# Kernel optimization log

Measured on AMD Instinct MI355X. Metric: run time of the kernel, lower is better.

The kernel has to match this reference:

```python
import jax, jax.numpy as jnp
import numpy as np

NUM_HEADS = 16
KEY_SIZE = 64
VALUE_SIZE = 64
D_MODEL = 1024
B, S = 2, 2048

def setup_inputs() -> dict:
    key = jax.random.key(0)
    k1, k2 = jax.random.split(key)
    inputs = jax.random.normal(k1, (B, S, D_MODEL), dtype=jnp.float32)
    qkv_width = NUM_HEADS * (KEY_SIZE + KEY_SIZE + VALUE_SIZE)  # 3072
    W = jax.random.normal(k2, (D_MODEL, qkv_width), dtype=jnp.float32) / np.sqrt(D_MODEL)
    b = jnp.zeros((qkv_width,), dtype=jnp.float32)
    return {"inputs": inputs, "W": W, "b": b}

def reference(inputs, W, b):
    # Fused QKV projection: [B, S, H*(2k+v)]
    qkv = jnp.einsum("bsd,de->bse", inputs, W) + b
    Bsz, S_ = inputs.shape[0], inputs.shape[1]
    qkv = qkv.reshape(Bsz, S_, NUM_HEADS, 2 * KEY_SIZE + VALUE_SIZE)
    qkv = jnp.transpose(qkv, (0, 2, 1, 3))  # [B, H, S, 2k+v]
    q = qkv[..., :KEY_SIZE]
    k = qkv[..., KEY_SIZE:2 * KEY_SIZE]
    v = qkv[..., 2 * KEY_SIZE:]
    # NOTE: original multiplies by sqrt(key_size) (not divide) -- faithful.
    scores = jnp.einsum("bhqd,bhkd->bhqk", q, k) * jnp.sqrt(jnp.float32(KEY_SIZE))
    weights = jax.nn.softmax(scores, axis=-1)
    out = jnp.einsum("bhqk,bhkv->bhqv", weights, v)  # [B, H, S, v]
    out = jnp.transpose(out, (0, 2, 1, 3)).reshape(Bsz, S_, NUM_HEADS * VALUE_SIZE)
    return out
```

## Files before the change

kernel.cpp:

```cpp
#include <hip/hip_runtime.h>


#define S_LEN 2048
#define NH    16
#define DH    64
#define DM    1024
#define EW    3072
#define NROWS 4096
#define NT    32

#define QSCALE 11.5415603f

using f32x4 = __attribute__((ext_vector_type(4))) float;
using bf8   = __attribute__((ext_vector_type(8))) short;
using s4v   = __attribute__((ext_vector_type(4))) short;

static __device__ __forceinline__ short f2bf(float f) {
  union { float f; unsigned u; } a; a.f = f;
  unsigned r = a.u + 0x7fffu + ((a.u >> 16) & 1u);
  return (short)(r >> 16);
}
static __device__ __forceinline__ float bf2f(short h) {
  union { float f; unsigned u; } a;
  a.u = ((unsigned)(unsigned short)h) << 16;
  return a.f;
}
static __device__ __forceinline__ void gl16(const void* g, void* l) {
  __builtin_amdgcn_global_load_lds(
      (const __attribute__((address_space(1))) void*)g,
      (__attribute__((address_space(3))) void*)l, 16, 0, 0);
}

__global__ __launch_bounds__(256) void prep_x(const float* __restrict__ X,
                                              short* __restrict__ Xh,
                                              short* __restrict__ Xl) {
  int i = blockIdx.x * 256 + threadIdx.x;
  float4 v = ((const float4*)X)[i];
  s4v h, l;
  h.x = f2bf(v.x); l.x = f2bf(v.x - bf2f(h.x));
  h.y = f2bf(v.y); l.y = f2bf(v.y - bf2f(h.y));
  h.z = f2bf(v.z); l.z = f2bf(v.z - bf2f(h.z));
  h.w = f2bf(v.w); l.w = f2bf(v.w - bf2f(h.w));
  ((s4v*)Xh)[i] = h;
  ((s4v*)Xl)[i] = l;
}

__global__ __launch_bounds__(256) void prep_w(const float* __restrict__ W,
                                              short* __restrict__ Wfh,
                                              short* __restrict__ Wfl) {
  __shared__ float t[32][33];
  int n0 = blockIdx.x * 32;
  int k0 = blockIdx.y * 32;
  int tx = threadIdx.x & 31;
  int ty = threadIdx.x >> 5;
#pragma unroll
  for (int i = 0; i < 32; i += 8)
    t[ty + i][tx] = W[(size_t)(k0 + ty + i) * EW + n0 + tx];
  __syncthreads();
  const int kt = k0 >> 5;
#pragma unroll
  for (int i = 0; i < 32; i += 8) {
    float v = t[tx][ty + i];
    int n = n0 + ty + i;
    int h = n / 192, e = n - h * 192;
    int np = (e < 64) ? (h * 64 + e)
           : (e < 128) ? (1024 + h * 64 + (e - 64))
                       : (2048 + h * 64 + (e - 128));
    int n16 = np >> 4, c = np & 15;
    int gg = (tx >> 3) & 3, ee = tx & 7;
    size_t o = ((size_t)(n16 * 32 + kt)) * 512 + (gg * 16 + c) * 8 + ee;
    short hi = f2bf(v);
    Wfh[o] = hi;
    if (np < 2048) Wfl[o] = f2bf(v - bf2f(hi));
  }
}

__global__ __launch_bounds__(256, 2) void proj_qk(
    const short* __restrict__ Xh, const short* __restrict__ Xl,
    const short* __restrict__ Wfh, const short* __restrict__ Wfl,
    const float* __restrict__ bias,
    short* __restrict__ Qh, short* __restrict__ Ql,
    short* __restrict__ Kh, short* __restrict__ Kl) {
  __shared__ short Ah[2][4096], Al[2][4096];
  const int tid = threadIdx.x;
  const int lane = tid & 63, w = tid >> 6;
  const int wr = w >> 1, wc = w & 1;
  const int c = lane & 15, g = lane >> 4;

  const int id = blockIdx.x;
  const int t = id >> 3;
  const int rowBase = (((id & 7) << 2) + (t & 3)) * 128;
  const int colBase = (t >> 2) * 128;

  f32x4 acc[4][4] = {};

  const int sr  = 32 * w + (lane >> 2);
  const int csw = ((lane & 3) ^ ((lane >> 3) & 3)) * 8;
  const int ldsw = w * 1024;
  const size_t aBase = (size_t)(rowBase + sr) * DM + csw;
  const int rsw = (g ^ ((c >> 1) & 3)) * 8;

  size_t bB[4];
#pragma unroll
  for (int n = 0; n < 4; ++n)
    bB[n] = ((size_t)((colBase >> 4) + wc * 4 + n) * 32) * 512 + lane * 8;

#define ASTAGE(B, kt) do {                                    \
    gl16(&Xh[aBase + (kt)],            &Ah[B][ldsw]);         \
    gl16(&Xh[aBase + (kt) + 16 * DM],  &Ah[B][ldsw + 512]);   \
    gl16(&Xl[aBase + (kt)],            &Al[B][ldsw]);         \
    gl16(&Xl[aBase + (kt) + 16 * DM],  &Al[B][ldsw + 512]);   \
  } while (0)
#define LOADB(dh, dl, kt) do {                                \
    _Pragma("unroll")                                         \
    for (int n = 0; n < 4; ++n) {                             \
      dh[n] = *(const bf8*)&Wfh[bB[n] + (size_t)(kt) * 512];  \
      dl[n] = *(const bf8*)&Wfl[bB[n] + (size_t)(kt) * 512];  \
    }                                                         \
  } while (0)
#define QKMFMA(bh, bl) do {                                   \
    _Pragma("unroll")                                         \
    for (int m = 0; m < 4; ++m) {                             \
      _Pragma("unroll")                                       \
      for (int n = 0; n < 4; ++n) {                           \
        acc[m][n] = __builtin_amdgcn_mfma_f32_16x16x32_bf16(al4[m], bh[n], acc[m][n], 0, 0, 0); \
        acc[m][n] = __builtin_amdgcn_mfma_f32_16x16x32_bf16(ah[m], bl[n], acc[m][n], 0, 0, 0);  \
        acc[m][n] = __builtin_amdgcn_mfma_f32_16x16x32_bf16(ah[m], bh[n], acc[m][n], 0, 0, 0);  \
      }                                                       \
    }                                                         \
  } while (0)

  bf8 b0h[4], b0l[4], b1h[4], b1l[4];
  LOADB(b0h, b0l, 0);
  ASTAGE(0, 0);
  __syncthreads();

  for (int it = 0; it < 32; it += 2) {
    LOADB(b1h, b1l, it + 1);
    bf8 ah[4], al4[4];
#pragma unroll
    for (int m = 0; m < 4; ++m) {
      int ro = (wr * 64 + m * 16 + c) * 32 + rsw;
      ah[m]  = *(const bf8*)&Ah[0][ro];
      al4[m] = *(const bf8*)&Al[0][ro];
    }
    ASTAGE(1, (it + 1) * 32);
    __builtin_amdgcn_s_setprio(1);
    QKMFMA(b0h, b0l);
    __builtin_amdgcn_s_setprio(0);
    __syncthreads();

    if (it + 2 < 32) LOADB(b0h, b0l, it + 2);
#pragma unroll
    for (int m = 0; m < 4; ++m) {
      int ro = (wr * 64 + m * 16 + c) * 32 + rsw;
      ah[m]  = *(const bf8*)&Ah[1][ro];
      al4[m] = *(const bf8*)&Al[1][ro];
    }
    if (it + 2 < 32) ASTAGE(0, (it + 2) * 32);
    __builtin_amdgcn_s_setprio(1);
    QKMFMA(b1h, b1l);
    __builtin_amdgcn_s_setprio(0);
    __syncthreads();
  }
#undef ASTAGE
#undef LOADB
#undef QKMFMA

#pragma unroll
  for (int m = 0; m < 4; ++m)
#pragma unroll
    for (int n = 0; n < 4; ++n)
#pragma unroll
      for (int j = 0; j < 4; ++j) {
        int grow = rowBase + wr * 64 + m * 16 + g * 4 + j;
        int gcol = colBase + wc * 64 + n * 16 + c;
        int h = (gcol >> 6) & 15, e = gcol & 63;
        int bb = grow >> 11, s = grow & 2047;
        size_t hb = (size_t)(bb * NH + h);
        if (gcol < 1024) {
          float q8 = (acc[m][n][j] + bias[h * 192 + e]) * QSCALE;
          short hi = f2bf(q8);
          short lo = f2bf(q8 - bf2f(hi));
          size_t idx = (hb * S_LEN + s) * DH + e;
          Qh[idx] = hi; Ql[idx] = lo;
        } else {
          float v = acc[m][n][j] + bias[h * 192 + 64 + e];
          short hi = f2bf(v);
          short lo = f2bf(v - bf2f(hi));
          int tile = s >> 6, r = s & 63;
          size_t idx = ((hb * NT + tile) * (size_t)4096) + r * 64 +
                       ((((e >> 3) ^ (r & 7)) << 3) | (e & 7));
          Kh[idx] = hi; Kl[idx] = lo;
        }
      }
}

__global__ __launch_bounds__(256, 2) void proj_v(
    const short* __restrict__ Xh, const short* __restrict__ Wfh,
    const float* __restrict__ bias, short* __restrict__ Vt) {
  __shared__ short Ah[2][4096];
  const int tid = threadIdx.x;
  const int lane = tid & 63, w = tid >> 6;
  const int wr = w >> 1, wc = w & 1;
  const int c = lane & 15, g = lane >> 4;

  const int id = blockIdx.x;
  const int t = id >> 3;
  const int rowBase = (((id & 7) << 2) + (t & 3)) * 128;
  const int colBase = 2048 + (t >> 2) * 128;

  f32x4 acc[4][4] = {};

  const int sr  = 32 * w + (lane >> 2);
  const int csw = ((lane & 3) ^ ((lane >> 3) & 3)) * 8;
  const int ldsw = w * 1024;
  const size_t aBase = (size_t)(rowBase + sr) * DM + csw;
  const int rsw = (g ^ ((c >> 1) & 3)) * 8;

  size_t bB[4];
#pragma unroll
  for (int n = 0; n < 4; ++n)
    bB[n] = ((size_t)((colBase >> 4) + wc * 4 + n) * 32) * 512 + lane * 8;

#define VASTAGE(B, kt) do {                                   \
    gl16(&Xh[aBase + (kt)],            &Ah[B][ldsw]);         \
    gl16(&Xh[aBase + (kt) + 16 * DM],  &Ah[B][ldsw + 512]);   \
  } while (0)
#define VLOADB(dh, kt) do {                                   \
    _Pragma("unroll")                                         \
    for (int n = 0; n < 4; ++n)                               \
      dh[n] = *(const bf8*)&Wfh[bB[n] + (size_t)(kt) * 512];  \
  } while (0)

  bf8 b0h[4], b1h[4];
  VLOADB(b0h, 0);
  VASTAGE(0, 0);
  __syncthreads();

  for (int it = 0; it < 32; it += 2) {
    VLOADB(b1h, it + 1);
    bf8 ah[4];
#pragma unroll
    for (int m = 0; m < 4; ++m)
      ah[m] = *(const bf8*)&Ah[0][(wr * 64 + m * 16 + c) * 32 + rsw];
    VASTAGE(1, (it + 1) * 32);
    __builtin_amdgcn_s_setprio(1);
#pragma unroll
    for (int m = 0; m < 4; ++m)
#pragma unroll
      for (int n = 0; n < 4; ++n)
        acc[m][n] = __builtin_amdgcn_mfma_f32_16x16x32_bf16(ah[m], b0h[n], acc[m][n], 0, 0, 0);
    __builtin_amdgcn_s_setprio(0);
    __syncthreads();

    if (it + 2 < 32) VLOADB(b0h, it + 2);
#pragma unroll
    for (int m = 0; m < 4; ++m)
      ah[m] = *(const bf8*)&Ah[1][(wr * 64 + m * 16 + c) * 32 + rsw];
    if (it + 2 < 32) VASTAGE(0, (it + 2) * 32);
    __builtin_amdgcn_s_setprio(1);
#pragma unroll
    for (int m = 0; m < 4; ++m)
#pragma unroll
      for (int n = 0; n < 4; ++n)
        acc[m][n] = __builtin_amdgcn_mfma_f32_16x16x32_bf16(ah[m], b1h[n], acc[m][n], 0, 0, 0);
    __builtin_amdgcn_s_setprio(0);
    __syncthreads();
  }
#undef VASTAGE
#undef VLOADB

#pragma unroll
  for (int m = 0; m < 4; ++m)
#pragma unroll
    for (int n = 0; n < 4; ++n)
#pragma unroll
      for (int j = 0; j < 4; ++j) {
        int grow = rowBase + wr * 64 + m * 16 + g * 4 + j;
        int gcol = colBase + wc * 64 + n * 16 + c;
        int h = (gcol >> 6) & 15, d = gcol & 63;
        int bb = grow >> 11, s = grow & 2047;
        size_t hb = (size_t)(bb * NH + h);
        float v = acc[m][n][j] + bias[h * 192 + 128 + d];
        int tile = s >> 6, key = s & 63;
        int kc = key >> 5, g4 = (key >> 2) & 3;
        int ii = (((key >> 4) & 1) << 2) | (key & 3);
        size_t idx = ((hb * NT + tile) * (size_t)4096) + d * 64 +
                     (((((kc << 2) | g4) ^ (d & 7)) << 3) | ii);
        Vt[idx] = f2bf(v);
      }
}

__global__ __launch_bounds__(512, 4) void attn(
    const short* __restrict__ Qh, const short* __restrict__ Ql,
    const short* __restrict__ KhG, const short* __restrict__ KlG,
    const short* __restrict__ VtG, float* __restrict__ out) {
  __shared__ short KHs[2][4096];
  __shared__ short KLs[2][4096];
  __shared__ short Vs[2][4096];

  const int tid = threadIdx.x;
  const int lane = tid & 63, w = tid >> 6;
  const int c = lane & 15, g = lane >> 4;
  const int id = blockIdx.x;
  const int lid = (id & 7) * 64 + (id >> 3);
  const int bh = lid >> 4;
  const int q0 = (lid & 15) * 128 + w * 16;
  const size_t qBase  = (size_t)bh * S_LEN * DH;
  const size_t kvBase = (size_t)bh * NT * 4096;

  const int seg = tid * 8;

  bf8 qh[2], ql[2];
#pragma unroll
  for (int kc = 0; kc < 2; ++kc) {
    size_t idx = qBase + (size_t)(q0 + c) * DH + kc * 32 + g * 8;
    qh[kc] = *(const bf8*)&Qh[idx];
    ql[kc] = *(const bf8*)&Ql[idx];
  }

  int koff[2][4];
#pragma unroll
  for (int kc = 0; kc < 2; ++kc)
#pragma unroll
    for (int i = 0; i < 4; ++i)
      koff[kc][i] = (i * 16 + c) * 64 + (((kc * 4 + g) ^ (c & 7)) << 3);

  f32x4 mneg = {0.f, 0.f, 0.f, 0.f};
  f32x4 osum = {};
  f32x4 o[4] = {};
  union { bf8 v; unsigned u[4]; } ones;
  ones.u[0] = ones.u[1] = ones.u[2] = ones.u[3] = 0x3F803F80u;

  gl16(&KhG[kvBase + seg], &KHs[0][seg]);
  gl16(&KlG[kvBase + seg], &KLs[0][seg]);
  gl16(&VtG[kvBase + seg], &Vs[0][seg]);
  __syncthreads();

  for (int t = 0; t < NT; ++t) {
    const int cur = t & 1, nxt = cur ^ 1;
    if (t + 1 < NT) {
      size_t tb = kvBase + (size_t)(t + 1) * 4096 + seg;
      gl16(&KhG[tb], &KHs[nxt][seg]);
      gl16(&KlG[tb], &KLs[nxt][seg]);
      gl16(&VtG[tb], &Vs[nxt][seg]);
    }
    const short* KH = &KHs[cur][0];
    const short* KL = &KLs[cur][0];
    const short* VV = &Vs[cur][0];

    f32x4 sc[4];
    __builtin_amdgcn_s_setprio(1);
#pragma unroll
    for (int nb = 0; nb < 4; ++nb) {
      bf8 kh0 = *(const bf8*)&KH[koff[0][nb]];
      bf8 kl0 = *(const bf8*)&KL[koff[0][nb]];
      f32x4 s = __builtin_amdgcn_mfma_f32_16x16x32_bf16(kh0, ql[0], mneg, 0, 0, 0);
      s = __builtin_amdgcn_mfma_f32_16x16x32_bf16(kl0, qh[0], s, 0, 0, 0);
      s = __builtin_amdgcn_mfma_f32_16x16x32_bf16(kh0, qh[0], s, 0, 0, 0);
      bf8 kh1 = *(const bf8*)&KH[koff[1][nb]];
      bf8 kl1 = *(const bf8*)&KL[koff[1][nb]];
      s = __builtin_amdgcn_mfma_f32_16x16x32_bf16(kh1, ql[1], s, 0, 0, 0);
      s = __builtin_amdgcn_mfma_f32_16x16x32_bf16(kl1, qh[1], s, 0, 0, 0);
      s = __builtin_amdgcn_mfma_f32_16x16x32_bf16(kh1, qh[1], s, 0, 0, 0);
      sc[nb] = s;
    }
    __builtin_amdgcn_s_setprio(0);

    float m0 = fmaxf(fmaxf(sc[0][0], sc[0][1]), sc[0][2]);
    m0 = fmaxf(fmaxf(m0, sc[0][3]), sc[1][0]);
    m0 = fmaxf(fmaxf(m0, sc[1][1]), sc[1][2]);
    m0 = fmaxf(fmaxf(m0, sc[1][3]), sc[2][0]);
    m0 = fmaxf(fmaxf(m0, sc[2][1]), sc[2][2]);
    m0 = fmaxf(fmaxf(m0, sc[2][3]), sc[3][0]);
    m0 = fmaxf(fmaxf(m0, sc[3][1]), sc[3][2]);
    m0 = fmaxf(m0, sc[3][3]);
    m0 = fmaxf(m0, __shfl_xor(m0, 16));
    m0 = fmaxf(m0, __shfl_xor(m0, 32));

    if (__any(m0 > 8.0f)) {
      float delta = fmaxf(m0, 0.0f);
      float scale = exp2f(-delta);
      int sb = (g << 4) | (g << 2);
      float s0 = __shfl(scale, sb);
      float s1 = __shfl(scale, sb + 1);
      float s2 = __shfl(scale, sb + 2);
      float s3 = __shfl(scale, sb + 3);
#pragma unroll
      for (int db = 0; db < 4; ++db) {
        o[db][0] *= s0; o[db][1] *= s1; o[db][2] *= s2; o[db][3] *= s3;
      }
      osum[0] *= s0; osum[1] *= s1; osum[2] *= s2; osum[3] *= s3;
      mneg[0] -= delta; mneg[1] -= delta; mneg[2] -= delta; mneg[3] -= delta;
#pragma unroll
      for (int nb = 0; nb < 4; ++nb)
#pragma unroll
        for (int j = 0; j < 4; ++j)
          sc[nb][j] = exp2f(sc[nb][j] - delta);
    } else {
#pragma unroll
      for (int nb = 0; nb < 4; ++nb)
#pragma unroll
        for (int j = 0; j < 4; ++j)
          sc[nb][j] = exp2f(sc[nb][j]);
    }

    union { bf8 v; unsigned u[4]; } pa[2];
#pragma unroll
    for (int kc = 0; kc < 2; ++kc) {
      asm("v_cvt_pk_bf16_f32 %0, %1, %2"
          : "=v"(pa[kc].u[0]) : "v"(sc[2 * kc][0]), "v"(sc[2 * kc][1]));
      asm("v_cvt_pk_bf16_f32 %0, %1, %2"
          : "=v"(pa[kc].u[1]) : "v"(sc[2 * kc][2]), "v"(sc[2 * kc][3]));
      asm("v_cvt_pk_bf16_f32 %0, %1, %2"
          : "=v"(pa[kc].u[2]) : "v"(sc[2 * kc + 1][0]), "v"(sc[2 * kc + 1][1]));
      asm("v_cvt_pk_bf16_f32 %0, %1, %2"
          : "=v"(pa[kc].u[3]) : "v"(sc[2 * kc + 1][2]), "v"(sc[2 * kc + 1][3]));
    }

    __builtin_amdgcn_s_setprio(1);
#pragma unroll
    for (int kc = 0; kc < 2; ++kc) {
      osum = __builtin_amdgcn_mfma_f32_16x16x32_bf16(pa[kc].v, ones.v, osum, 0, 0, 0);
#pragma unroll
      for (int db = 0; db < 4; ++db) {
        bf8 vb = *(const bf8*)&VV[koff[kc][db]];
        o[db] = __builtin_amdgcn_mfma_f32_16x16x32_bf16(pa[kc].v, vb, o[db], 0, 0, 0);
      }
    }
    __builtin_amdgcn_s_setprio(0);

    __syncthreads();
  }

  float r0 = 1.f / osum[0];
  float r1 = 1.f / osum[1];
  float r2 = 1.f / osum[2];
  float r3 = 1.f / osum[3];

  const int b = bh >> 4, h = bh & 15;
#pragma unroll
  for (int db = 0; db < 4; ++db) {
    int col = h * DH + db * 16 + c;
    out[((size_t)b * S_LEN + q0 + g * 4 + 0) * DM + col] = o[db][0] * r0;
    out[((size_t)b * S_LEN + q0 + g * 4 + 1) * DM + col] = o[db][1] * r1;
    out[((size_t)b * S_LEN + q0 + g * 4 + 2) * DM + col] = o[db][2] * r2;
    out[((size_t)b * S_LEN + q0 + g * 4 + 3) * DM + col] = o[db][3] * r3;
  }
}

extern "C" void kernel_launch(void* const* d_in, const int* in_sizes, int n_in,
                              void* d_out, int out_size, void* d_ws, size_t ws_size,
                              hipStream_t stream) {
  const float* X    = (const float*)d_in[0];
  const float* W    = (const float*)d_in[1];
  const float* bias = (const float*)d_in[2];
  float* out = (float*)d_out;

  char* ws = (char*)d_ws;
  size_t off = 0;
  auto take = [&](size_t bytes) {
    void* p = ws + off;
    off += (bytes + 255) & ~(size_t)255;
    return p;
  };
  short* Xh  = (short*)take((size_t)NROWS * DM * 2);
  short* Xl  = (short*)take((size_t)NROWS * DM * 2);
  short* Wfh = (short*)take((size_t)EW * DM * 2);
  short* Wfl = (short*)take((size_t)EW * DM * 2);
  short* Qh  = (short*)take((size_t)2 * NH * S_LEN * DH * 2);
  short* Ql  = (short*)take((size_t)2 * NH * S_LEN * DH * 2);
  short* Kh  = (short*)take((size_t)2 * NH * NT * 4096 * 2);
  short* Kl  = (short*)take((size_t)2 * NH * NT * 4096 * 2);
  short* Vt  = (short*)take((size_t)2 * NH * NT * 4096 * 2);

  prep_x<<<dim3(4096), dim3(256), 0, stream>>>(X, Xh, Xl);
  prep_w<<<dim3(EW / 32, DM / 32), dim3(256), 0, stream>>>(W, Wfh, Wfl);
  proj_qk<<<dim3(512), dim3(256), 0, stream>>>(
      Xh, Xl, Wfh, Wfl, bias, Qh, Ql, Kh, Kl);
  proj_v<<<dim3(256), dim3(256), 0, stream>>>(Xh, Wfh, bias, Vt);
  attn<<<dim3(512), dim3(512), 0, stream>>>(
      Qh, Ql, Kh, Kl, Vt, out);
}
```

Measured before the change: 174.4 us.

## Merge QK and V projections into one launch; load V directly from global

```diff
diff --git a/kernel.cpp b/kernel.cpp
--- a/kernel.cpp
+++ b/kernel.cpp
@@ -75,35 +75,37 @@
   }
 }
 
-__global__ __launch_bounds__(256, 2) void proj_qk(
+__global__ __launch_bounds__(256, 2) void proj(
     const short* __restrict__ Xh, const short* __restrict__ Xl,
     const short* __restrict__ Wfh, const short* __restrict__ Wfl,
     const float* __restrict__ bias,
     short* __restrict__ Qh, short* __restrict__ Ql,
-    short* __restrict__ Kh, short* __restrict__ Kl) {
+    short* __restrict__ Kh, short* __restrict__ Kl,
+    short* __restrict__ Vt) {
   __shared__ short Ah[2][4096], Al[2][4096];
   const int tid = threadIdx.x;
   const int lane = tid & 63, w = tid >> 6;
   const int wr = w >> 1, wc = w & 1;
   const int c = lane & 15, g = lane >> 4;
 
-  const int id = blockIdx.x;
-  const int t = id >> 3;
-  const int rowBase = (((id & 7) << 2) + (t & 3)) * 128;
-  const int colBase = (t >> 2) * 128;
-
-  f32x4 acc[4][4] = {};
-
   const int sr  = 32 * w + (lane >> 2);
   const int csw = ((lane & 3) ^ ((lane >> 3) & 3)) * 8;
   const int ldsw = w * 1024;
-  const size_t aBase = (size_t)(rowBase + sr) * DM + csw;
   const int rsw = (g ^ ((c >> 1) & 3)) * 8;
 
-  size_t bB[4];
-#pragma unroll
-  for (int n = 0; n < 4; ++n)
-    bB[n] = ((size_t)((colBase >> 4) + wc * 4 + n) * 32) * 512 + lane * 8;
+  if (blockIdx.x < 512) {
+    const int id = blockIdx.x;
+    const int t = id >> 3;
+    const int rowBase = (((id & 7) << 2) + (t & 3)) * 128;
+    const int colBase = (t >> 2) * 128;
+
+    f32x4 acc[4][4] = {};
+    const size_t aBase = (size_t)(rowBase + sr) * DM + csw;
+
+    size_t bB[4];
+#pragma unroll
+    for (int n = 0; n < 4; ++n)
+      bB[n] = ((size_t)((colBase >> 4) + wc * 4 + n) * 32) * 512 + lane * 8;
 
 #define ASTAGE(B, kt) do {                                    \
     gl16(&Xh[aBase + (kt)],            &Ah[B][ldsw]);         \
@@ -130,98 +132,83 @@
     }                                                         \
   } while (0)
 
-  bf8 b0h[4], b0l[4], b1h[4], b1l[4];
-  LOADB(b0h, b0l, 0);
-  ASTAGE(0, 0);
-  __syncthreads();
-
-  for (int it = 0; it < 32; it += 2) {
-    LOADB(b1h, b1l, it + 1);
-    bf8 ah[4], al4[4];
-#pragma unroll
-    for (int m = 0; m < 4; ++m) {
-      int ro = (wr * 64 + m * 16 + c) * 32 + rsw;
-      ah[m]  = *(const bf8*)&Ah[0][ro];
-      al4[m] = *(const bf8*)&Al[0][ro];
-    }
-    ASTAGE(1, (it + 1) * 32);
-    __builtin_amdgcn_s_setprio(1);
-    QKMFMA(b0h, b0l);
-    __builtin_amdgcn_s_setprio(0);
+    bf8 b0h[4], b0l[4], b1h[4], b1l[4];
+    LOADB(b0h, b0l, 0);
+    ASTAGE(0, 0);
     __syncthreads();
 
-    if (it + 2 < 32) LOADB(b0h, b0l, it + 2);
-#pragma unroll
-    for (int m = 0; m < 4; ++m) {
-      int ro = (wr * 64 + m * 16 + c) * 32 + rsw;
-      ah[m]  = *(const bf8*)&Ah[1][ro];
-      al4[m] = *(const bf8*)&Al[1][ro];
-    }
-    if (it + 2 < 32) ASTAGE(0, (it + 2) * 32);
-    __builtin_amdgcn_s_setprio(1);
-    QKMFMA(b1h, b1l);
-    __builtin_amdgcn_s_setprio(0);
-    __syncthreads();
-  }
+    for (int it = 0; it < 32; it += 2) {
+      LOADB(b1h, b1l, it + 1);
+      bf8 ah[4], al4[4];
+#pragma unroll
+      for (int m = 0; m < 4; ++m) {
+        int ro = (wr * 64 + m * 16 + c) * 32 + rsw;
+        ah[m]  = *(const bf8*)&Ah[0][ro];
+        al4[m] = *(const bf8*)&Al[0][ro];
+      }
+      ASTAGE(1, (it + 1) * 32);
+      __builtin_amdgcn_s_setprio(1);
+      QKMFMA(b0h, b0l);
+      __builtin_amdgcn_s_setprio(0);
+      __syncthreads();
+
+      if (it + 2 < 32) LOADB(b0h, b0l, it + 2);
+#pragma unroll
+      for (int m = 0; m < 4; ++m) {
+        int ro = (wr * 64 + m * 16 + c) * 32 + rsw;
+        ah[m]  = *(const bf8*)&Ah[1][ro];
+        al4[m] = *(const bf8*)&Al[1][ro];
+      }
+      if (it + 2 < 32) ASTAGE(0, (it + 2) * 32);
+      __builtin_amdgcn_s_setprio(1);
+      QKMFMA(b1h, b1l);
+      __builtin_amdgcn_s_setprio(0);
+      __syncthreads();
+    }
 #undef ASTAGE
 #undef LOADB
 #undef QKMFMA
 
 #pragma unroll
-  for (int m = 0; m < 4; ++m)
+    for (int m = 0; m < 4; ++m)
+#pragma unroll
+      for (int n = 0; n < 4; ++n)
+#pragma unroll
+        for (int j = 0; j < 4; ++j) {
+          int grow = rowBase + wr * 64 + m * 16 + g * 4 + j;
+          int gcol = colBase + wc * 64 + n * 16 + c;
+          int h = (gcol >> 6) & 15, e = gcol & 63;
+          int bb = grow >> 11, s = grow & 2047;
+          size_t hb = (size_t)(bb * NH + h);
+          if (gcol < 1024) {
+            float q8 = (acc[m][n][j] + bias[h * 192 + e]) * QSCALE;
+            short hi = f2bf(q8);
+            short lo = f2bf(q8 - bf2f(hi));
+            size_t idx = (hb * S_LEN + s) * DH + e;
+            Qh[idx] = hi; Ql[idx] = lo;
+          } else {
+            float v = acc[m][n][j] + bias[h * 192 + 64 + e];
+            short hi = f2bf(v);
+            short lo = f2bf(v - bf2f(hi));
+            int tile = s >> 6, r = s & 63;
+            size_t idx = ((hb * NT + tile) * (size_t)4096) + r * 64 +
+                         ((((e >> 3) ^ (r & 7)) << 3) | (e & 7));
+            Kh[idx] = hi; Kl[idx] = lo;
+          }
+        }
+  } else {
+    const int id = blockIdx.x - 512;
+    const int t = id >> 3;
+    const int rowBase = (((id & 7) << 2) + (t & 3)) * 128;
+    const int colBase = 2048 + (t >> 2) * 128;
+
+    f32x4 acc[4][4] = {};
+    const size_t aBase = (size_t)(rowBase + sr) * DM + csw;
+
+    size_t bB[4];
 #pragma unroll
     for (int n = 0; n < 4; ++n)
-#pragma unroll
-      for (int j = 0; j < 4; ++j) {
-        int grow = rowBase + wr * 64 + m * 16 + g * 4 + j;
-        int gcol = colBase + wc * 64 + n * 16 + c;
-        int h = (gcol >> 6) & 15, e = gcol & 63;
-        int bb = grow >> 11, s = grow & 2047;
-        size_t hb = (size_t)(bb * NH + h);
-        if (gcol < 1024) {
-          float q8 = (acc[m][n][j] + bias[h * 192 + e]) * QSCALE;
-          short hi = f2bf(q8);
-          short lo = f2bf(q8 - bf2f(hi));
-          size_t idx = (hb * S_LEN + s) * DH + e;
-          Qh[idx] = hi; Ql[idx] = lo;
-        } else {
-          float v = acc[m][n][j] + bias[h * 192 + 64 + e];
-          short hi = f2bf(v);
-          short lo = f2bf(v - bf2f(hi));
-          int tile = s >> 6, r = s & 63;
-          size_t idx = ((hb * NT + tile) * (size_t)4096) + r * 64 +
-                       ((((e >> 3) ^ (r & 7)) << 3) | (e & 7));
-          Kh[idx] = hi; Kl[idx] = lo;
-        }
-      }
-}
-
-__global__ __launch_bounds__(256, 2) void proj_v(
-    const short* __restrict__ Xh, const short* __restrict__ Wfh,
-    const float* __restrict__ bias, short* __restrict__ Vt) {
-  __shared__ short Ah[2][4096];
-  const int tid = threadIdx.x;
-  const int lane = tid & 63, w = tid >> 6;
-  const int wr = w >> 1, wc = w & 1;
-  const int c = lane & 15, g = lane >> 4;
-
-  const int id = blockIdx.x;
-  const int t = id >> 3;
-  const int rowBase = (((id & 7) << 2) + (t & 3)) * 128;
-  const int colBase = 2048 + (t >> 2) * 128;
-
-  f32x4 acc[4][4] = {};
-
-  const int sr  = 32 * w + (lane >> 2);
-  const int csw = ((lane & 3) ^ ((lane >> 3) & 3)) * 8;
-  const int ldsw = w * 1024;
-  const size_t aBase = (size_t)(rowBase + sr) * DM + csw;
-  const int rsw = (g ^ ((c >> 1) & 3)) * 8;
-
-  size_t bB[4];
-#pragma unroll
-  for (int n = 0; n < 4; ++n)
-    bB[n] = ((size_t)((colBase >> 4) + wc * 4 + n) * 32) * 512 + lane * 8;
+      bB[n] = ((size_t)((colBase >> 4) + wc * 4 + n) * 32) * 512 + lane * 8;
 
 #define VASTAGE(B, kt) do {                                   \
     gl16(&Xh[aBase + (kt)],            &Ah[B][ldsw]);         \
@@ -233,63 +220,64 @@
       dh[n] = *(const bf8*)&Wfh[bB[n] + (size_t)(kt) * 512];  \
   } while (0)
 
-  bf8 b0h[4], b1h[4];
-  VLOADB(b0h, 0);
-  VASTAGE(0, 0);
-  __syncthreads();
-
-  for (int it = 0; it < 32; it += 2) {
-    VLOADB(b1h, it + 1);
-    bf8 ah[4];
-#pragma unroll
-    for (int m = 0; m < 4; ++m)
-      ah[m] = *(const bf8*)&Ah[0][(wr * 64 + m * 16 + c) * 32 + rsw];
-    VASTAGE(1, (it + 1) * 32);
-    __builtin_amdgcn_s_setprio(1);
-#pragma unroll
-    for (int m = 0; m < 4; ++m)
-#pragma unroll
-      for (int n = 0; n < 4; ++n)
-        acc[m][n] = __builtin_amdgcn_mfma_f32_16x16x32_bf16(ah[m], b0h[n], acc[m][n], 0, 0, 0);
-    __builtin_amdgcn_s_setprio(0);
+    bf8 b0h[4], b1h[4];
+    VLOADB(b0h, 0);
+    VASTAGE(0, 0);
     __syncthreads();
 
-    if (it + 2 < 32) VLOADB(b0h, it + 2);
-#pragma unroll
-    for (int m = 0; m < 4; ++m)
-      ah[m] = *(const bf8*)&Ah[1][(wr * 64 + m * 16 + c) * 32 + rsw];
-    if (it + 2 < 32) VASTAGE(0, (it + 2) * 32);
-    __builtin_amdgcn_s_setprio(1);
-#pragma unroll
-    for (int m = 0; m < 4; ++m)
-#pragma unroll
-      for (int n = 0; n < 4; ++n)
-        acc[m][n] = __builtin_amdgcn_mfma_f32_16x16x32_bf16(ah[m], b1h[n], acc[m][n], 0, 0, 0);
-    __builtin_amdgcn_s_setprio(0);
-    __syncthreads();
-  }
+    for (int it = 0; it < 32; it += 2) {
+      VLOADB(b1h, it + 1);
+      bf8 ah[4];
+#pragma unroll
+      for (int m = 0; m < 4; ++m)
+        ah[m] = *(const bf8*)&Ah[0][(wr * 64 + m * 16 + c) * 32 + rsw];
+      VASTAGE(1, (it + 1) * 32);
+      __builtin_amdgcn_s_setprio(1);
+#pragma unroll
+      for (int m = 0; m < 4; ++m)
+#pragma unroll
+        for (int n = 0; n < 4; ++n)
+          acc[m][n] = __builtin_amdgcn_mfma_f32_16x16x32_bf16(ah[m], b0h[n], acc[m][n], 0, 0, 0);
+      __builtin_amdgcn_s_setprio(0);
+      __syncthreads();
+
+      if (it + 2 < 32) VLOADB(b0h, it + 2);
+#pragma unroll
+      for (int m = 0; m < 4; ++m)
+        ah[m] = *(const bf8*)&Ah[1][(wr * 64 + m * 16 + c) * 32 + rsw];
+      if (it + 2 < 32) VASTAGE(0, (it + 2) * 32);
+      __builtin_amdgcn_s_setprio(1);
+#pragma unroll
+      for (int m = 0; m < 4; ++m)
+#pragma unroll
+        for (int n = 0; n < 4; ++n)
+          acc[m][n] = __builtin_amdgcn_mfma_f32_16x16x32_bf16(ah[m], b1h[n], acc[m][n], 0, 0, 0);
+      __builtin_amdgcn_s_setprio(0);
+      __syncthreads();
+    }
 #undef VASTAGE
 #undef VLOADB
 
 #pragma unroll
-  for (int m = 0; m < 4; ++m)
-#pragma unroll
-    for (int n = 0; n < 4; ++n)
-#pragma unroll
-      for (int j = 0; j < 4; ++j) {
-        int grow = rowBase + wr * 64 + m * 16 + g * 4 + j;
-        int gcol = colBase + wc * 64 + n * 16 + c;
-        int h = (gcol >> 6) & 15, d = gcol & 63;
-        int bb = grow >> 11, s = grow & 2047;
-        size_t hb = (size_t)(bb * NH + h);
-        float v = acc[m][n][j] + bias[h * 192 + 128 + d];
-        int tile = s >> 6, key = s & 63;
-        int kc = key >> 5, g4 = (key >> 2) & 3;
-        int ii = (((key >> 4) & 1) << 2) | (key & 3);
-        size_t idx = ((hb * NT + tile) * (size_t)4096) + d * 64 +
-                     (((((kc << 2) | g4) ^ (d & 7)) << 3) | ii);
-        Vt[idx] = f2bf(v);
-      }
+    for (int m = 0; m < 4; ++m)
+#pragma unroll
+      for (int n = 0; n < 4; ++n)
+#pragma unroll
+        for (int j = 0; j < 4; ++j) {
+          int grow = rowBase + wr * 64 + m * 16 + g * 4 + j;
+          int gcol = colBase + wc * 64 + n * 16 + c;
+          int h = (gcol >> 6) & 15, d = gcol & 63;
+          int bb = grow >> 11, s = grow & 2047;
+          size_t hb = (size_t)(bb * NH + h);
+          float v = acc[m][n][j] + bias[h * 192 + 128 + d];
+          int tile = s >> 6, key = s & 63;
+          int kc = key >> 5, g4 = (key >> 2) & 3;
+          int ii = (((key >> 4) & 1) << 2) | (key & 3);
+          size_t idx = ((hb * NT + tile) * (size_t)4096) + d * 64 +
+                       ((((kc << 2) | g4) << 3) | ii);
+          Vt[idx] = f2bf(v);
+        }
+  }
 }
 
 __global__ __launch_bounds__(512, 4) void attn(
@@ -298,7 +286,6 @@
     const short* __restrict__ VtG, float* __restrict__ out) {
   __shared__ short KHs[2][4096];
   __shared__ short KLs[2][4096];
-  __shared__ short Vs[2][4096];
 
   const int tid = threadIdx.x;
   const int lane = tid & 63, w = tid >> 6;
@@ -327,6 +314,13 @@
     for (int i = 0; i < 4; ++i)
       koff[kc][i] = (i * 16 + c) * 64 + (((kc * 4 + g) ^ (c & 7)) << 3);
 
+  int voff[2][4];
+#pragma unroll
+  for (int kc = 0; kc < 2; ++kc)
+#pragma unroll
+    for (int db = 0; db < 4; ++db)
+      voff[kc][db] = (db * 16 + c) * 64 + (kc * 4 + g) * 8;
+
   f32x4 mneg = {0.f, 0.f, 0.f, 0.f};
   f32x4 osum = {};
   f32x4 o[4] = {};
@@ -335,20 +329,26 @@
 
   gl16(&KhG[kvBase + seg], &KHs[0][seg]);
   gl16(&KlG[kvBase + seg], &KLs[0][seg]);
-  gl16(&VtG[kvBase + seg], &Vs[0][seg]);
   __syncthreads();
 
   for (int t = 0; t < NT; ++t) {
     const int cur = t & 1, nxt = cur ^ 1;
+    const size_t vtb = kvBase + (size_t)t * 4096;
+
+    bf8 vb[2][4];
+#pragma unroll
+    for (int kc = 0; kc < 2; ++kc)
+#pragma unroll
+      for (int db = 0; db < 4; ++db)
+        vb[kc][db] = *(const bf8*)&VtG[vtb + voff[kc][db]];
+
     if (t + 1 < NT) {
       size_t tb = kvBase + (size_t)(t + 1) * 4096 + seg;
       gl16(&KhG[tb], &KHs[nxt][seg]);
       gl16(&KlG[tb], &KLs[nxt][seg]);
-      gl16(&VtG[tb], &Vs[nxt][seg]);
     }
     const short* KH = &KHs[cur][0];
     const short* KL = &KLs[cur][0];
-    const short* VV = &Vs[cur][0];
 
     f32x4 sc[4];
     __builtin_amdgcn_s_setprio(1);
@@ -424,10 +424,8 @@
     for (int kc = 0; kc < 2; ++kc) {
       osum = __builtin_amdgcn_mfma_f32_16x16x32_bf16(pa[kc].v, ones.v, osum, 0, 0, 0);
 #pragma unroll
-      for (int db = 0; db < 4; ++db) {
-        bf8 vb = *(const bf8*)&VV[koff[kc][db]];
-        o[db] = __builtin_amdgcn_mfma_f32_16x16x32_bf16(pa[kc].v, vb, o[db], 0, 0, 0);
-      }
+      for (int db = 0; db < 4; ++db)
+        o[db] = __builtin_amdgcn_mfma_f32_16x16x32_bf16(pa[kc].v, vb[kc][db], o[db], 0, 0, 0);
     }
     __builtin_amdgcn_s_setprio(0);
 
@@ -477,9 +475,8 @@
 
   prep_x<<<dim3(4096), dim3(256), 0, stream>>>(X, Xh, Xl);
   prep_w<<<dim3(EW / 32, DM / 32), dim3(256), 0, stream>>>(W, Wfh, Wfl);
-  proj_qk<<<dim3(512), dim3(256), 0, stream>>>(
-      Xh, Xl, Wfh, Wfl, bias, Qh, Ql, Kh, Kl);
-  proj_v<<<dim3(256), dim3(256), 0, stream>>>(Xh, Wfh, bias, Vt);
+  proj<<<dim3(768), dim3(256), 0, stream>>>(
+      Xh, Xl, Wfh, Wfl, bias, Qh, Ql, Kh, Kl, Vt);
   attn<<<dim3(512), dim3(512), 0, stream>>>(
       Qh, Ql, Kh, Kl, Vt, out);
 }
```

After: 328.7 us. 88.5% more time.

## Process two 16-row query blocks per wave in attention to reuse K/V tiles

Applied to the files above, without the earlier changes.

```diff
diff --git a/kernel.cpp b/kernel.cpp
--- a/kernel.cpp
+++ b/kernel.cpp
@@ -292,7 +292,7 @@
       }
 }
 
-__global__ __launch_bounds__(512, 4) void attn(
+__global__ __launch_bounds__(512, 2) void attn(
     const short* __restrict__ Qh, const short* __restrict__ Ql,
     const short* __restrict__ KhG, const short* __restrict__ KlG,
     const short* __restrict__ VtG, float* __restrict__ out) {
@@ -304,21 +304,23 @@
   const int lane = tid & 63, w = tid >> 6;
   const int c = lane & 15, g = lane >> 4;
   const int id = blockIdx.x;
-  const int lid = (id & 7) * 64 + (id >> 3);
-  const int bh = lid >> 4;
-  const int q0 = (lid & 15) * 128 + w * 16;
+  const int lid = (id & 7) * 32 + (id >> 3);
+  const int bh = lid >> 3;
+  const int q0 = (lid & 7) * 256 + w * 32;
   const size_t qBase  = (size_t)bh * S_LEN * DH;
   const size_t kvBase = (size_t)bh * NT * 4096;
 
   const int seg = tid * 8;
 
-  bf8 qh[2], ql[2];
-#pragma unroll
-  for (int kc = 0; kc < 2; ++kc) {
-    size_t idx = qBase + (size_t)(q0 + c) * DH + kc * 32 + g * 8;
-    qh[kc] = *(const bf8*)&Qh[idx];
-    ql[kc] = *(const bf8*)&Ql[idx];
-  }
+  bf8 qh[2][2], ql[2][2];
+#pragma unroll
+  for (int rb = 0; rb < 2; ++rb)
+#pragma unroll
+    for (int kc = 0; kc < 2; ++kc) {
+      size_t idx = qBase + (size_t)(q0 + rb * 16 + c) * DH + kc * 32 + g * 8;
+      qh[rb][kc] = *(const bf8*)&Qh[idx];
+      ql[rb][kc] = *(const bf8*)&Ql[idx];
+    }
 
   int koff[2][4];
 #pragma unroll
@@ -327,9 +329,9 @@
     for (int i = 0; i < 4; ++i)
       koff[kc][i] = (i * 16 + c) * 64 + (((kc * 4 + g) ^ (c & 7)) << 3);
 
-  f32x4 mneg = {0.f, 0.f, 0.f, 0.f};
-  f32x4 osum = {};
-  f32x4 o[4] = {};
+  f32x4 mneg0 = {0.f, 0.f, 0.f, 0.f}, mneg1 = {0.f, 0.f, 0.f, 0.f};
+  f32x4 osum0 = {}, osum1 = {};
+  f32x4 o0[4] = {}, o1[4] = {};
   union { bf8 v; unsigned u[4]; } ones;
   ones.u[0] = ones.u[1] = ones.u[2] = ones.u[3] = 0x3F803F80u;
 
@@ -350,83 +352,132 @@
     const short* KL = &KLs[cur][0];
     const short* VV = &Vs[cur][0];
 
-    f32x4 sc[4];
+    f32x4 sc0[4], sc1[4];
     __builtin_amdgcn_s_setprio(1);
 #pragma unroll
     for (int nb = 0; nb < 4; ++nb) {
       bf8 kh0 = *(const bf8*)&KH[koff[0][nb]];
       bf8 kl0 = *(const bf8*)&KL[koff[0][nb]];
-      f32x4 s = __builtin_amdgcn_mfma_f32_16x16x32_bf16(kh0, ql[0], mneg, 0, 0, 0);
-      s = __builtin_amdgcn_mfma_f32_16x16x32_bf16(kl0, qh[0], s, 0, 0, 0);
-      s = __builtin_amdgcn_mfma_f32_16x16x32_bf16(kh0, qh[0], s, 0, 0, 0);
+      f32x4 s0 = __builtin_amdgcn_mfma_f32_16x16x32_bf16(kh0, ql[0][0], mneg0, 0, 0, 0);
+      s0 = __builtin_amdgcn_mfma_f32_16x16x32_bf16(kl0, qh[0][0], s0, 0, 0, 0);
+      s0 = __builtin_amdgcn_mfma_f32_16x16x32_bf16(kh0, qh[0][0], s0, 0, 0, 0);
+      f32x4 s1 = __builtin_amdgcn_mfma_f32_16x16x32_bf16(kh0, ql[1][0], mneg1, 0, 0, 0);
+      s1 = __builtin_amdgcn_mfma_f32_16x16x32_bf16(kl0, qh[1][0], s1, 0, 0, 0);
+      s1 = __builtin_amdgcn_mfma_f32_16x16x32_bf16(kh0, qh[1][0], s1, 0, 0, 0);
       bf8 kh1 = *(const bf8*)&KH[koff[1][nb]];
       bf8 kl1 = *(const bf8*)&KL[koff[1][nb]];
-      s = __builtin_amdgcn_mfma_f32_16x16x32_bf16(kh1, ql[1], s, 0, 0, 0);
-      s = __builtin_amdgcn_mfma_f32_16x16x32_bf16(kl1, qh[1], s, 0, 0, 0);
-      s = __builtin_amdgcn_mfma_f32_16x16x32_bf16(kh1, qh[1], s, 0, 0, 0);
-      sc[nb] = s;
+      s0 = __builtin_amdgcn_mfma_f32_16x16x32_bf16(kh1, ql[0][1], s0, 0, 0, 0);
+      s0 = __builtin_amdgcn_mfma_f32_16x16x32_bf16(kl1, qh[0][1], s0, 0, 0, 0);
+      s0 = __builtin_amdgcn_mfma_f32_16x16x32_bf16(kh1, qh[0][1], s0, 0, 0, 0);
+      s1 = __builtin_amdgcn_mfma_f32_16x16x32_bf16(kh1, ql[1][1], s1, 0, 0, 0);
+      s1 = __builtin_amdgcn_mfma_f32_16x16x32_bf16(kl1, qh[1][1], s1, 0, 0, 0);
+      s1 = __builtin_amdgcn_mfma_f32_16x16x32_bf16(kh1, qh[1][1], s1, 0, 0, 0);
+      sc0[nb] = s0; sc1[nb] = s1;
     }
     __builtin_amdgcn_s_setprio(0);
 
-    float m0 = fmaxf(fmaxf(sc[0][0], sc[0][1]), sc[0][2]);
-    m0 = fmaxf(fmaxf(m0, sc[0][3]), sc[1][0]);
-    m0 = fmaxf(fmaxf(m0, sc[1][1]), sc[1][2]);
-    m0 = fmaxf(fmaxf(m0, sc[1][3]), sc[2][0]);
-    m0 = fmaxf(fmaxf(m0, sc[2][1]), sc[2][2]);
-    m0 = fmaxf(fmaxf(m0, sc[2][3]), sc[3][0]);
-    m0 = fmaxf(fmaxf(m0, sc[3][1]), sc[3][2]);
-    m0 = fmaxf(m0, sc[3][3]);
-    m0 = fmaxf(m0, __shfl_xor(m0, 16));
-    m0 = fmaxf(m0, __shfl_xor(m0, 32));
-
-    if (__any(m0 > 8.0f)) {
-      float delta = fmaxf(m0, 0.0f);
-      float scale = exp2f(-delta);
+    float m00 = fmaxf(fmaxf(sc0[0][0], sc0[0][1]), sc0[0][2]);
+    m00 = fmaxf(fmaxf(m00, sc0[0][3]), sc0[1][0]);
+    m00 = fmaxf(fmaxf(m00, sc0[1][1]), sc0[1][2]);
+    m00 = fmaxf(fmaxf(m00, sc0[1][3]), sc0[2][0]);
+    m00 = fmaxf(fmaxf(m00, sc0[2][1]), sc0[2][2]);
+    m00 = fmaxf(fmaxf(m00, sc0[2][3]), sc0[3][0]);
+    m00 = fmaxf(fmaxf(m00, sc0[3][1]), sc0[3][2]);
+    m00 = fmaxf(m00, sc0[3][3]);
+    m00 = fmaxf(m00, __shfl_xor(m00, 16));
+    m00 = fmaxf(m00, __shfl_xor(m00, 32));
+    float m01 = fmaxf(fmaxf(sc1[0][0], sc1[0][1]), sc1[0][2]);
+    m01 = fmaxf(fmaxf(m01, sc1[0][3]), sc1[1][0]);
+    m01 = fmaxf(fmaxf(m01, sc1[1][1]), sc1[1][2]);
+    m01 = fmaxf(fmaxf(m01, sc1[1][3]), sc1[2][0]);
+    m01 = fmaxf(fmaxf(m01, sc1[2][1]), sc1[2][2]);
+    m01 = fmaxf(fmaxf(m01, sc1[2][3]), sc1[3][0]);
+    m01 = fmaxf(fmaxf(m01, sc1[3][1]), sc1[3][2]);
+    m01 = fmaxf(m01, sc1[3][3]);
+    m01 = fmaxf(m01, __shfl_xor(m01, 16));
+    m01 = fmaxf(m01, __shfl_xor(m01, 32));
+
+    if (__any(fmaxf(m00, m01) > 8.0f)) {
       int sb = (g << 4) | (g << 2);
-      float s0 = __shfl(scale, sb);
-      float s1 = __shfl(scale, sb + 1);
-      float s2 = __shfl(scale, sb + 2);
-      float s3 = __shfl(scale, sb + 3);
-#pragma unroll
-      for (int db = 0; db < 4; ++db) {
-        o[db][0] *= s0; o[db][1] *= s1; o[db][2] *= s2; o[db][3] *= s3;
+      {
+        float delta = fmaxf(m00, 0.0f);
+        float scale = exp2f(-delta);
+        float s0 = __shfl(scale, sb);
+        float s1 = __shfl(scale, sb + 1);
+        float s2 = __shfl(scale, sb + 2);
+        float s3 = __shfl(scale, sb + 3);
+#pragma unroll
+        for (int db = 0; db < 4; ++db) {
+          o0[db][0] *= s0; o0[db][1] *= s1; o0[db][2] *= s2; o0[db][3] *= s3;
+        }
+        osum0[0] *= s0; osum0[1] *= s1; osum0[2] *= s2; osum0[3] *= s3;
+        mneg0[0] -= delta; mneg0[1] -= delta; mneg0[2] -= delta; mneg0[3] -= delta;
+#pragma unroll
+        for (int nb = 0; nb < 4; ++nb)
+#pragma unroll
+          for (int j = 0; j < 4; ++j)
+            sc0[nb][j] = exp2f(sc0[nb][j] - delta);
       }
-      osum[0] *= s0; osum[1] *= s1; osum[2] *= s2; osum[3] *= s3;
-      mneg[0] -= delta; mneg[1] -= delta; mneg[2] -= delta; mneg[3] -= delta;
+      {
+        float delta = fmaxf(m01, 0.0f);
+        float scale = exp2f(-delta);
+        float s0 = __shfl(scale, sb);
+        float s1 = __shfl(scale, sb + 1);
+        float s2 = __shfl(scale, sb + 2);
+        float s3 = __shfl(scale, sb + 3);
+#pragma unroll
+        for (int db = 0; db < 4; ++db) {
+          o1[db][0] *= s0; o1[db][1] *= s1; o1[db][2] *= s2; o1[db][3] *= s3;
+        }
+        osum1[0] *= s0; osum1[1] *= s1; osum1[2] *= s2; osum1[3] *= s3;
+        mneg1[0] -= delta; mneg1[1] -= delta; mneg1[2] -= delta; mneg1[3] -= delta;
+#pragma unroll
+        for (int nb = 0; nb < 4; ++nb)
+#pragma unroll
+          for (int j = 0; j < 4; ++j)
+            sc1[nb][j] = exp2f(sc1[nb][j] - delta);
+      }
+    } else {
 #pragma unroll
       for (int nb = 0; nb < 4; ++nb)
 #pragma unroll
-        for (int j = 0; j < 4; ++j)
-          sc[nb][j] = exp2f(sc[nb][j] - delta);
-    } else {
-#pragma unroll
-      for (int nb = 0; nb < 4; ++nb)
-#pragma unroll
-        for (int j = 0; j < 4; ++j)
-          sc[nb][j] = exp2f(sc[nb][j]);
-    }
-
-    union { bf8 v; unsigned u[4]; } pa[2];
+        for (int j = 0; j < 4; ++j) {
+          sc0[nb][j] = exp2f(sc0[nb][j]);
+          sc1[nb][j] = exp2f(sc1[nb][j]);
+        }
+    }
+
+    union { bf8 v; unsigned u[4]; } pa0[2], pa1[2];
 #pragma unroll
     for (int kc = 0; kc < 2; ++kc) {
       asm("v_cvt_pk_bf16_f32 %0, %1, %2"
-          : "=v"(pa[kc].u[0]) : "v"(sc[2 * kc][0]), "v"(sc[2 * kc][1]));
-      asm("v_cvt_pk_bf16_f32 %0, %1, %2"
-          : "=v"(pa[kc].u[1]) : "v"(sc[2 * kc][2]), "v"(sc[2 * kc][3]));
-      asm("v_cvt_pk_bf16_f32 %0, %1, %2"
-          : "=v"(pa[kc].u[2]) : "v"(sc[2 * kc + 1][0]), "v"(sc[2 * kc + 1][1]));
-      asm("v_cvt_pk_bf16_f32 %0, %1, %2"
-          : "=v"(pa[kc].u[3]) : "v"(sc[2 * kc + 1][2]), "v"(sc[2 * kc + 1][3]));
+          : "=v"(pa0[kc].u[0]) : "v"(sc0[2 * kc][0]), "v"(sc0[2 * kc][1]));
+      asm("v_cvt_pk_bf16_f32 %0, %1, %2"
+          : "=v"(pa0[kc].u[1]) : "v"(sc0[2 * kc][2]), "v"(sc0[2 * kc][3]));
+      asm("v_cvt_pk_bf16_f32 %0, %1, %2"
+          : "=v"(pa0[kc].u[2]) : "v"(sc0[2 * kc + 1][0]), "v"(sc0[2 * kc + 1][1]));
+      asm("v_cvt_pk_bf16_f32 %0, %1, %2"
+          : "=v"(pa0[kc].u[3]) : "v"(sc0[2 * kc + 1][2]), "v"(sc0[2 * kc + 1][3]));
+      asm("v_cvt_pk_bf16_f32 %0, %1, %2"
+          : "=v"(pa1[kc].u[0]) : "v"(sc1[2 * kc][0]), "v"(sc1[2 * kc][1]));
+      asm("v_cvt_pk_bf16_f32 %0, %1, %2"
+          : "=v"(pa1[kc].u[1]) : "v"(sc1[2 * kc][2]), "v"(sc1[2 * kc][3]));
+      asm("v_cvt_pk_bf16_f32 %0, %1, %2"
+          : "=v"(pa1[kc].u[2]) : "v"(sc1[2 * kc + 1][0]), "v"(sc1[2 * kc + 1][1]));
+      asm("v_cvt_pk_bf16_f32 %0, %1, %2"
+          : "=v"(pa1[kc].u[3]) : "v"(sc1[2 * kc + 1][2]), "v"(sc1[2 * kc + 1][3]));
     }
 
     __builtin_amdgcn_s_setprio(1);
 #pragma unroll
     for (int kc = 0; kc < 2; ++kc) {
-      osum = __builtin_amdgcn_mfma_f32_16x16x32_bf16(pa[kc].v, ones.v, osum, 0, 0, 0);
+      osum0 = __builtin_amdgcn_mfma_f32_16x16x32_bf16(pa0[kc].v, ones.v, osum0, 0, 0, 0);
+      osum1 = __builtin_amdgcn_mfma_f32_16x16x32_bf16(pa1[kc].v, ones.v, osum1, 0, 0, 0);
 #pragma unroll
       for (int db = 0; db < 4; ++db) {
         bf8 vb = *(const bf8*)&VV[koff[kc][db]];
-        o[db] = __builtin_amdgcn_mfma_f32_16x16x32_bf16(pa[kc].v, vb, o[db], 0, 0, 0);
+        o0[db] = __builtin_amdgcn_mfma_f32_16x16x32_bf16(pa0[kc].v, vb, o0[db], 0, 0, 0);
+        o1[db] = __builtin_amdgcn_mfma_f32_16x16x32_bf16(pa1[kc].v, vb, o1[db], 0, 0, 0);
       }
     }
     __builtin_amdgcn_s_setprio(0);
@@ -434,19 +485,26 @@
     __syncthreads();
   }
 
-  float r0 = 1.f / osum[0];
-  float r1 = 1.f / osum[1];
-  float r2 = 1.f / osum[2];
-  float r3 = 1.f / osum[3];
-
   const int b = bh >> 4, h = bh & 15;
 #pragma unroll
   for (int db = 0; db < 4; ++db) {
     int col = h * DH + db * 16 + c;
-    out[((size_t)b * S_LEN + q0 + g * 4 + 0) * DM + col] = o[db][0] * r0;
-    out[((size_t)b * S_LEN + q0 + g * 4 + 1) * DM + col] = o[db][1] * r1;
-    out[((size_t)b * S_LEN + q0 + g * 4 + 2) * DM + col] = o[db][2] * r2;
-    out[((size_t)b * S_LEN + q0 + g * 4 + 3) * DM + col] = o[db][3] * r3;
+    {
+      float r0 = 1.f / osum0[0], r1 = 1.f / osum0[1];
+      float r2 = 1.f / osum0[2], r3 = 1.f / osum0[3];
+      out[((size_t)b * S_LEN + q0 + g * 4 + 0) * DM + col] = o0[db][0] * r0;
+      out[((size_t)b * S_LEN + q0 + g * 4 + 1) * DM + col] = o0[db][1] * r1;
+      out[((size_t)b * S_LEN + q0 + g * 4 + 2) * DM + col] = o0[db][2] * r2;
+      out[((size_t)b * S_LEN + q0 + g * 4 + 3) * DM + col] = o0[db][3] * r3;
+    }
+    {
+      float r0 = 1.f / osum1[0], r1 = 1.f / osum1[1];
+      float r2 = 1.f / osum1[2], r3 = 1.f / osum1[3];
+      out[((size_t)b * S_LEN + q0 + 16 + g * 4 + 0) * DM + col] = o1[db][0] * r0;
+      out[((size_t)b * S_LEN + q0 + 16 + g * 4 + 1) * DM + col] = o1[db][1] * r1;
+      out[((size_t)b * S_LEN + q0 + 16 + g * 4 + 2) * DM + col] = o1[db][2] * r2;
+      out[((size_t)b * S_LEN + q0 + 16 + g * 4 + 3) * DM + col] = o1[db][3] * r3;
+    }
   }
 }
 
@@ -480,6 +538,6 @@
   proj_qk<<<dim3(512), dim3(256), 0, stream>>>(
       Xh, Xl, Wfh, Wfl, bias, Qh, Ql, Kh, Kl);
   proj_v<<<dim3(256), dim3(256), 0, stream>>>(Xh, Wfh, bias, Vt);
-  attn<<<dim3(512), dim3(512), 0, stream>>>(
+  attn<<<dim3(256), dim3(512), 0, stream>>>(
       Qh, Ql, Kh, Kl, Vt, out);
 }
```

New measurement: 181.9 us. +4.3%, slower.
